# Performance work log

Measured on AMD Instinct MI355X. Metric: run time of the kernel, lower is better.

Reference implementation:

```python
import jax, jax.numpy as jnp
import numpy as np

B, N, D, H = 1, 4096, 512, 8
HD = D // H


def setup_inputs() -> dict:
    key = jax.random.key(0)
    ks = jax.random.split(key, 12)
    s = 0.02  # weight init scale for numerical stability
    query = jax.random.normal(ks[0], (B, N, D), jnp.float32)
    key_t = jax.random.normal(ks[1], (B, N, D), jnp.float32)
    value = jax.random.normal(ks[2], (B, N, D), jnp.float32)
    Wq = jax.random.normal(ks[3], (D, D), jnp.float32) * s
    bq = jax.random.normal(ks[4], (D,), jnp.float32) * s
    Wk = jax.random.normal(ks[5], (D, D), jnp.float32) * s
    bk = jax.random.normal(ks[6], (D,), jnp.float32) * s
    Wv = jax.random.normal(ks[7], (D, D), jnp.float32) * s
    bv = jax.random.normal(ks[8], (D,), jnp.float32) * s
    Wo = jax.random.normal(ks[9], (D, D), jnp.float32) * s
    bo = jax.random.normal(ks[10], (D,), jnp.float32) * s
    # build sgconv_mat exactly as __init__: shifted nonneg adjacency, max-normalized,
    # then symmetric degree normalization D^-1/2 A D^-1/2 (gwmha_layer_num=1)
    A = jax.random.uniform(ks[11], (N, N), jnp.float32)
    A = A + A.min()
    A = A / A.max()
    deg = A.sum(1)
    dinv = 1.0 / jnp.sqrt(deg)
    sgconv_mat = (dinv[:, None] * A * dinv[None, :])[None]  # [1,N,N]
    return {"query": query, "key": key_t, "value": value,
            "Wq": Wq, "bq": bq, "Wk": Wk, "bk": bk, "Wv": Wv, "bv": bv,
            "Wo": Wo, "bo": bo, "sgconv_mat": sgconv_mat}


def reference(query, key, value, Wq, bq, Wk, bk, Wv, bv, Wo, bo, sgconv_mat):
    b, n, d = query.shape
    q = (query @ Wq.T + bq).reshape(b, n, H, HD)
    k = (key @ Wk.T + bk).reshape(b, n, H, HD)
    v = (value @ Wv.T + bv).reshape(b, n, H, HD)
    energy = jnp.einsum('bqhd,bkhd->bhqk', q, k)
    attn = jax.nn.softmax(energy / jnp.sqrt(jnp.float32(d)), axis=3)
    out = jnp.einsum('bhqk,bkhd->bqhd', attn, v).reshape(b, n, d)
    out = sgconv_mat @ out          # [1,N,N] @ [B,N,D] -> [B,N,D]
    return out @ Wo.T + bo
```

## Files before the change

### kernel.cpp

```cpp
#include <hip/hip_runtime.h>
#include <hip/hip_bf16.h>
#include <math.h>

typedef __bf16 bf16_t;
typedef __bf16 bf16x8 __attribute__((ext_vector_type(8)));
typedef float floatx4 __attribute__((ext_vector_type(4)));

typedef __attribute__((address_space(1))) void gvoid_t;
typedef __attribute__((address_space(3))) void lvoid_t;

static __device__ __forceinline__ void gload_lds16(const bf16_t* g, const bf16_t* l) {
    __builtin_amdgcn_global_load_lds((gvoid_t*)(size_t)g,
                                     (lvoid_t*)(unsigned)(size_t)l,
                                     16, 0, 0);
}

static __device__ __forceinline__ unsigned pack_bf2(float lo, float hi) {
    bf16_t a = (bf16_t)lo, b = (bf16_t)hi;
    return (unsigned)__builtin_bit_cast(unsigned short, a)
         | ((unsigned)__builtin_bit_cast(unsigned short, b) << 16);
}

static __device__ inline void store_c(float* C, size_t i, float v) { C[i] = v; }
static __device__ inline void store_c(bf16_t* C, size_t i, float v) { C[i] = (bf16_t)v; }

static __device__ inline void cvt8(const float* src, bf16_t* dst, size_t idx) {
    float4 a = *(const float4*)(src + idx);
    float4 c = *(const float4*)(src + idx + 4);
    uint4 u;
    u.x = pack_bf2(a.x, a.y);
    u.y = pack_bf2(a.z, a.w);
    u.z = pack_bf2(c.x, c.y);
    u.w = pack_bf2(c.z, c.w);
    *(uint4*)(dst + idx) = u;
}

template <typename TC>
__device__ inline void gemm_body128(
    const bf16_t* __restrict__ A, int lda,
    const bf16_t* __restrict__ B, int ldb,
    const float* __restrict__ bias_col, const float* __restrict__ bias_row,
    float cscale,
    TC* __restrict__ C, int ldc, int K, int m0, int n0)
{
    __shared__ bf16_t As[128 * 32];
    __shared__ bf16_t Bs[128 * 32];

    const int tid = threadIdx.x;
    const int lane = tid & 63, wave = tid >> 6;
    const int wm = wave & 1, wn = wave >> 1;
    const int lo16 = lane & 15, quad = lane >> 4;

    const int r0 = tid >> 2;
    const int s0 = tid & 3;
    const int c0 = s0 ^ ((r0 >> 1) & 3);
    const bf16_t* ga0 = A + (size_t)(m0 + r0) * lda + c0 * 8;
    const bf16_t* ga1 = A + (size_t)(m0 + 64 + r0) * lda + c0 * 8;
    const bf16_t* gb0 = B + (size_t)(n0 + r0) * ldb + c0 * 8;
    const bf16_t* gb1 = B + (size_t)(n0 + 64 + r0) * ldb + c0 * 8;
    const bf16_t* la0 = As + wave * 512;
    const bf16_t* la1 = As + 2048 + wave * 512;
    const bf16_t* lb0 = Bs + wave * 512;
    const bf16_t* lb1 = Bs + 2048 + wave * 512;

    int aoff[4], boff[4];
#pragma unroll
    for (int t = 0; t < 4; ++t) {
        const int ra = wm * 64 + t * 16 + lo16;
        aoff[t] = ra * 32 + ((quad ^ ((ra >> 1) & 3)) << 3);
        const int rb = wn * 64 + t * 16 + lo16;
        boff[t] = rb * 32 + ((quad ^ ((rb >> 1) & 3)) << 3);
    }

    floatx4 acc[4][4] = {};

    for (int k0 = 0; k0 < K; k0 += 32) {
        __syncthreads();
        gload_lds16(ga0 + k0, la0);
        gload_lds16(ga1 + k0, la1);
        gload_lds16(gb0 + k0, lb0);
        gload_lds16(gb1 + k0, lb1);
        __syncthreads();

        bf16x8 af[4], bfv[4];
#pragma unroll
        for (int t = 0; t < 4; ++t) {
            af[t]  = *(const bf16x8*)(As + aoff[t]);
            bfv[t] = *(const bf16x8*)(Bs + boff[t]);
        }
        __builtin_amdgcn_s_setprio(1);
#pragma unroll
        for (int mt = 0; mt < 4; ++mt)
#pragma unroll
            for (int nt = 0; nt < 4; ++nt)
                acc[mt][nt] = __builtin_amdgcn_mfma_f32_16x16x32_bf16(
                    af[mt], bfv[nt], acc[mt][nt], 0, 0, 0);
        __builtin_amdgcn_s_setprio(0);
    }

#pragma unroll
    for (int nt = 0; nt < 4; ++nt) {
        const int gn = n0 + wn * 64 + nt * 16 + lo16;
        const float bc = bias_col ? bias_col[gn] : 0.f;
#pragma unroll
        for (int mt = 0; mt < 4; ++mt) {
#pragma unroll
            for (int r = 0; r < 4; ++r) {
                const int gm = m0 + wm * 64 + mt * 16 + quad * 4 + r;
                float v = acc[mt][nt][r] + bc;
                if (bias_row) v += bias_row[gm];
                store_c(C, (size_t)gm * ldc + gn, v * cscale);
            }
        }
    }
}

__global__ __launch_bounds__(256) void prep(
    const float* __restrict__ query, const float* __restrict__ key, const float* __restrict__ value,
    const float* __restrict__ Wq, const float* __restrict__ Wk,
    const float* __restrict__ Wv, const float* __restrict__ Wo,
    bf16_t* qB, bf16_t* kB, bf16_t* vB,
    bf16_t* wqB, bf16_t* wkB, bf16_t* wvB, bf16_t* woB)
{
    const int b = blockIdx.x;
    const float* src; bf16_t* dst; size_t base;
    if      (b < 256) { src = query; dst = qB;  base = (size_t)b * 8192; }
    else if (b < 512) { src = key;   dst = kB;  base = (size_t)(b - 256) * 8192; }
    else if (b < 768) { src = value; dst = vB;  base = (size_t)(b - 512) * 8192; }
    else if (b < 800) { src = Wq;    dst = wqB; base = (size_t)(b - 768) * 8192; }
    else if (b < 832) { src = Wk;    dst = wkB; base = (size_t)(b - 800) * 8192; }
    else if (b < 864) { src = Wv;    dst = wvB; base = (size_t)(b - 832) * 8192; }
    else              { src = Wo;    dst = woB; base = (size_t)(b - 864) * 8192; }
#pragma unroll
    for (int it = 0; it < 4; ++it)
        cvt8(src, dst, base + (size_t)it * 2048 + threadIdx.x * 8);
}

__global__ __launch_bounds__(256) void proj_qkv(
    const bf16_t* __restrict__ qB, const bf16_t* __restrict__ wqB, const float* __restrict__ bq,
    const bf16_t* __restrict__ kB, const bf16_t* __restrict__ wkB, const float* __restrict__ bk,
    const bf16_t* __restrict__ wvB, const bf16_t* __restrict__ vB, const float* __restrict__ bv,
    bf16_t* __restrict__ q, bf16_t* __restrict__ k, bf16_t* __restrict__ vt, float qscale,
    const float* __restrict__ sg, bf16_t* __restrict__ sgb)
{
    const int b = blockIdx.x;
    if (b >= 384) {
        const size_t base = (size_t)(b - 384) * 8192;
#pragma unroll
        for (int it = 0; it < 4; ++it)
            cvt8(sg, sgb, base + (size_t)it * 2048 + threadIdx.x * 8);
        return;
    }
    const int i = b & 127;
    if (b < 256) {
        const int m0 = (i & 31) * 128, n0 = (i >> 5) * 128;
        if (b < 128)
            gemm_body128<bf16_t>(qB, 512, wqB, 512, bq, nullptr, qscale, q, 512, 512, m0, n0);
        else
            gemm_body128<bf16_t>(kB, 512, wkB, 512, bk, nullptr, 1.f, k, 512, 512, m0, n0);
    } else {
        const int m0 = (i & 3) * 128, n0 = (i >> 2) * 128;
        gemm_body128<bf16_t>(wvB, 512, vB, 512, nullptr, bv, 1.f, vt, 4096, 512, m0, n0);
    }
}

__global__ __launch_bounds__(256) void sgconv_gemm(
    const bf16_t* __restrict__ sgb, const bf16_t* __restrict__ aot,
    float* __restrict__ part)
{
    const int i = blockIdx.x & 127;
    const int kb = blockIdx.x >> 7;
    const int m0 = (i & 31) * 128, n0 = (i >> 5) * 128;
    const int kbase = kb * 512;
    gemm_body128<float>(sgb + kbase, 4096, aot + kbase, 4096, nullptr, nullptr, 1.f,
                        part + (size_t)kb * (4096 * 512), 512, 512, m0, n0);
}

__global__ __launch_bounds__(256) void part_reduce(
    const float* __restrict__ p, bf16_t* __restrict__ o2)
{
    const size_t S = (size_t)4096 * 512;
    const size_t idx = ((size_t)blockIdx.x * 256 + threadIdx.x) * 8;
    uint4 u;
#pragma unroll
    for (int half = 0; half < 2; ++half) {
        float4 s = *(const float4*)(p + idx + half * 4);
#pragma unroll
        for (int kb = 1; kb < 8; ++kb) {
            float4 t = *(const float4*)(p + kb * S + idx + half * 4);
            s.x += t.x; s.y += t.y; s.z += t.z; s.w += t.w;
        }
        if (half == 0) { u.x = pack_bf2(s.x, s.y); u.y = pack_bf2(s.z, s.w); }
        else           { u.z = pack_bf2(s.x, s.y); u.w = pack_bf2(s.z, s.w); }
    }
    *(uint4*)(o2 + idx) = u;
}

__global__ __launch_bounds__(256) void out_proj(
    const bf16_t* __restrict__ o2, const bf16_t* __restrict__ woB,
    const float* __restrict__ bo, float* __restrict__ out)
{
    const int i = blockIdx.x, x = i & 7, t = i >> 3;
    const int n0 = (t & 7) * 64;
    const int m0 = ((t >> 3) * 8 + x) * 64;

    __shared__ bf16_t As[64 * 68];
    __shared__ bf16_t Bs[64 * 68];

    const int tid = threadIdx.x;
    const int lane = tid & 63, wave = tid >> 6;
    const int wm = wave & 1, wn = wave >> 1;
    const int lo16 = lane & 15, quad = lane >> 4;
    const int sr = tid >> 2, sc = (tid & 3) * 8;

    floatx4 acc[2][2] = {};

    for (int k0 = 0; k0 < 512; k0 += 32) {
        bf16x8 a0 = *(const bf16x8*)(o2 + (size_t)(m0 + sr) * 512 + k0 + sc);
        bf16x8 b0 = *(const bf16x8*)(woB + (size_t)(n0 + sr) * 512 + k0 + sc);
        __syncthreads();
        *(bf16x8*)(&As[sr * 68 + sc]) = a0;
        *(bf16x8*)(&Bs[sr * 68 + sc]) = b0;
        __syncthreads();

        bf16x8 af[2], bfv[2];
#pragma unroll
        for (int mt = 0; mt < 2; ++mt)
            af[mt] = *(const bf16x8*)(&As[(wm * 32 + mt * 16 + lo16) * 68 + quad * 8]);
#pragma unroll
        for (int nt = 0; nt < 2; ++nt)
            bfv[nt] = *(const bf16x8*)(&Bs[(wn * 32 + nt * 16 + lo16) * 68 + quad * 8]);
#pragma unroll
        for (int mt = 0; mt < 2; ++mt)
#pragma unroll
            for (int nt = 0; nt < 2; ++nt)
                acc[mt][nt] = __builtin_amdgcn_mfma_f32_16x16x32_bf16(
                    af[mt], bfv[nt], acc[mt][nt], 0, 0, 0);
    }

#pragma unroll
    for (int nt = 0; nt < 2; ++nt) {
        const int gn = n0 + wn * 32 + nt * 16 + lo16;
        const float bc = bo[gn];
#pragma unroll
        for (int mt = 0; mt < 2; ++mt)
#pragma unroll
            for (int r = 0; r < 4; ++r) {
                const int gm = m0 + wm * 32 + mt * 16 + quad * 4 + r;
                out[(size_t)gm * 512 + gn] = acc[mt][nt][r] + bc;
            }
    }
}

__global__ __launch_bounds__(256, 4) void flash_attn(
    const bf16_t* __restrict__ q, const bf16_t* __restrict__ kk,
    const bf16_t* __restrict__ vt, float* __restrict__ op,
    float* __restrict__ lp)
{
    const int fid = blockIdx.x;

    const int N = 4096, D = 512;
    const int h   = fid & 7;
    const int qb  = (fid >> 3) & 31;
    const int qtr = fid >> 8;
    const int t0  = qtr * 1024;

    const int tid = threadIdx.x;
    const int w = tid >> 6, lane = tid & 63;
    const int lo16 = lane & 15, quad = lane >> 4;

    __shared__ bf16_t Ks[64 * 72];
    __shared__ bf16_t Vs[64 * 72];
    __shared__ bf16_t Ps[4][32 * 72];

    const bf16_t* qp = q + (size_t)(qb * 128 + w * 32 + lo16) * D + h * 64 + quad * 8;
    bf16x8 qf[2][2];
    qf[0][0] = *(const bf16x8*)qp;
    qf[0][1] = *(const bf16x8*)(qp + 32);
    qf[1][0] = *(const bf16x8*)(qp + 16 * D);
    qf[1][1] = *(const bf16x8*)(qp + 16 * D + 32);

    const int srow = tid >> 2, sc = (tid & 3) * 16;
    const bf16_t* ksrc = kk + (size_t)(t0 + srow) * D + h * 64 + sc;
    const bf16_t* vsrc = vt + (size_t)(h * 64 + srow) * N + t0 + sc;
    bf16_t* kdst = &Ks[srow * 72 + sc];
    bf16_t* vdst = &Vs[srow * 72 + sc];

    bf16x8 ones;
#pragma unroll
    for (int i = 0; i < 8; ++i) ones[i] = (bf16_t)1.0f;

    floatx4 o[4][2] = {};
    floatx4 lacc[2] = {};

    bf16x8 kr0 = *(const bf16x8*)ksrc;
    bf16x8 kr1 = *(const bf16x8*)(ksrc + 8);
    bf16x8 vr0 = *(const bf16x8*)vsrc;
    bf16x8 vr1 = *(const bf16x8*)(vsrc + 8);

    for (int it = 0; it < 16; ++it) {
        __syncthreads();
        *(bf16x8*)kdst = kr0;  *(bf16x8*)(kdst + 8) = kr1;
        *(bf16x8*)vdst = vr0;  *(bf16x8*)(vdst + 8) = vr1;
        __syncthreads();
        if (it < 15) {
            const bf16_t* kn = ksrc + (size_t)(it + 1) * 64 * D;
            const bf16_t* vn = vsrc + (it + 1) * 64;
            kr0 = *(const bf16x8*)kn;  kr1 = *(const bf16x8*)(kn + 8);
            vr0 = *(const bf16x8*)vn;  vr1 = *(const bf16x8*)(vn + 8);
        }

        floatx4 s[4][2];
        __builtin_amdgcn_s_setprio(1);
#pragma unroll
        for (int tt = 0; tt < 4; ++tt) {
            bf16x8 kf0 = *(const bf16x8*)(&Ks[(tt * 16 + lo16) * 72 + quad * 8]);
            bf16x8 kf1 = *(const bf16x8*)(&Ks[(tt * 16 + lo16) * 72 + 32 + quad * 8]);
#pragma unroll
            for (int qt = 0; qt < 2; ++qt) {
                floatx4 a = {};
                a = __builtin_amdgcn_mfma_f32_16x16x32_bf16(kf0, qf[qt][0], a, 0, 0, 0);
                a = __builtin_amdgcn_mfma_f32_16x16x32_bf16(kf1, qf[qt][1], a, 0, 0, 0);
                s[tt][qt] = a;
            }
        }
        __builtin_amdgcn_s_setprio(0);
#pragma unroll
        for (int tt = 0; tt < 4; ++tt)
#pragma unroll
            for (int qt = 0; qt < 2; ++qt) {
                float e0 = __builtin_amdgcn_exp2f(s[tt][qt][0]);
                float e1 = __builtin_amdgcn_exp2f(s[tt][qt][1]);
                float e2 = __builtin_amdgcn_exp2f(s[tt][qt][2]);
                float e3 = __builtin_amdgcn_exp2f(s[tt][qt][3]);
                uint2 pk;
                pk.x = pack_bf2(e0, e1);
                pk.y = pack_bf2(e2, e3);
                *(uint2*)(&Ps[w][(qt * 16 + lo16) * 72 + tt * 16 + quad * 4]) = pk;
            }
        __builtin_amdgcn_s_setprio(1);
#pragma unroll
        for (int ks = 0; ks < 2; ++ks) {
            bf16x8 pf0 = *(const bf16x8*)(&Ps[w][lo16 * 72 + ks * 32 + quad * 8]);
            bf16x8 pf1 = *(const bf16x8*)(&Ps[w][(16 + lo16) * 72 + ks * 32 + quad * 8]);
            lacc[0] = __builtin_amdgcn_mfma_f32_16x16x32_bf16(ones, pf0, lacc[0], 0, 0, 0);
            lacc[1] = __builtin_amdgcn_mfma_f32_16x16x32_bf16(ones, pf1, lacc[1], 0, 0, 0);
#pragma unroll
            for (int t = 0; t < 4; ++t) {
                bf16x8 vf = *(const bf16x8*)(&Vs[(t * 16 + lo16) * 72 + ks * 32 + quad * 8]);
                o[t][0] = __builtin_amdgcn_mfma_f32_16x16x32_bf16(vf, pf0, o[t][0], 0, 0, 0);
                o[t][1] = __builtin_amdgcn_mfma_f32_16x16x32_bf16(vf, pf1, o[t][1], 0, 0, 0);
            }
        }
        __builtin_amdgcn_s_setprio(0);
    }

    const int g = fid & 255;
    float* opw = op + ((size_t)qtr * 256 + g) * 8192;
#pragma unroll
    for (int t = 0; t < 4; ++t)
#pragma unroll
        for (int pt = 0; pt < 2; ++pt)
#pragma unroll
            for (int r = 0; r < 4; ++r)
                opw[(t * 16 + quad * 4 + r) * 128 + w * 32 + pt * 16 + lo16] = o[t][pt][r];

    if (quad == 0) {
        float* lpw = lp + ((size_t)qtr * 256 + g) * 128;
        lpw[w * 32 + lo16] = lacc[0][0];
        lpw[w * 32 + 16 + lo16] = lacc[1][0];
    }
}

__global__ __launch_bounds__(256) void attn_combine(
    const float* __restrict__ op, const float* __restrict__ lp, bf16_t* __restrict__ aot)
{
    const int bid = blockIdx.x;
    const int g = bid >> 2, qu = bid & 3;
    const int h = g & 7, qb = g >> 3;
    const int tid = threadIdx.x;
    __shared__ float ls[128];
    if (tid < 128) {
        float s = 0.f;
#pragma unroll
        for (int qtr = 0; qtr < 4; ++qtr)
            s += lp[((size_t)qtr * 256 + g) * 128 + tid];
        ls[tid] = 1.0f / s;
    }
    __syncthreads();
    const float* b0 = op + (size_t)g * 8192;
    const size_t QS = (size_t)256 * 8192;
#pragma unroll
    for (int i = 0; i < 8; ++i) {
        int idx = qu * 2048 + i * 256 + tid;
        float v = b0[idx] + b0[QS + idx] + b0[2 * QS + idx] + b0[3 * QS + idx];
        int dim = idx >> 7, qc = idx & 127;
        aot[(size_t)(h * 64 + dim) * 4096 + qb * 128 + qc] = (bf16_t)(v * ls[qc]);
    }
}

extern "C" void kernel_launch(void* const* d_in, const int* in_sizes, int n_in,
                              void* d_out, int out_size, void* d_ws, size_t ws_size,
                              hipStream_t stream)
{
    const int N = 4096, D = 512;
    const float* query = (const float*)d_in[0];
    const float* key_t = (const float*)d_in[1];
    const float* value = (const float*)d_in[2];
    const float* Wq = (const float*)d_in[3];
    const float* bq = (const float*)d_in[4];
    const float* Wk = (const float*)d_in[5];
    const float* bk = (const float*)d_in[6];
    const float* Wv = (const float*)d_in[7];
    const float* bv = (const float*)d_in[8];
    const float* Wo = (const float*)d_in[9];
    const float* bo = (const float*)d_in[10];
    const float* sg = (const float*)d_in[11];
    float* out = (float*)d_out;

    const size_t ND = (size_t)N * D;
    const size_t DD = (size_t)D * D;

    char* base = (char*)d_ws;
    bf16_t* q    = (bf16_t*)base;
    bf16_t* kk   = q   + ND;
    bf16_t* vt   = kk  + ND;
    bf16_t* aot  = vt  + ND;
    bf16_t* sgb  = aot + ND;
    char* regA   = (char*)(sgb + (size_t)N * N);
    bf16_t* qB   = (bf16_t*)regA;
    bf16_t* kB   = qB + ND;
    bf16_t* vB   = kB + ND;
    bf16_t* wqB  = vB + ND;
    bf16_t* wkB  = wqB + DD;
    bf16_t* wvB  = wkB + DD;
    float* op    = (float*)regA;
    float* p     = (float*)regA;
    char* tail   = regA + (size_t)8 * (4096 * 512) * 4;
    float*  lp   = (float*)tail;
    bf16_t* woB  = (bf16_t*)(lp + (size_t)4 * 256 * 128);
    bf16_t* o2   = woB + DD;

    const dim3 blk(256);

    prep<<<896, blk, 0, stream>>>(query, key_t, value, Wq, Wk, Wv, Wo,
                                  qB, kB, vB, wqB, wkB, wvB, woB);

    const float qscale = 1.44269504088896f / sqrtf((float)D);
    proj_qkv<<<2432, blk, 0, stream>>>(qB, wqB, bq, kB, wkB, bk,
                                       wvB, vB, bv, q, kk, vt, qscale, sg, sgb);

    flash_attn<<<1024, blk, 0, stream>>>(q, kk, vt, op, lp);
    attn_combine<<<1024, blk, 0, stream>>>(op, lp, aot);

    sgconv_gemm<<<1024, blk, 0, stream>>>(sgb, aot, p);
    part_reduce<<<1024, blk, 0, stream>>>(p, o2);
    out_proj<<<512, blk, 0, stream>>>(o2, woB, bo, out);

    (void)in_sizes; (void)n_in; (void)out_size; (void)ws_size;
}
```

Before: 261.3 us.

## Replace split-K sgconv GEMM and reduction with single full-K 64x64 kernel

The sgconv matmul used to be split-K over 8 slices. Each slice wrote fp32 partials and a separate reduce kernel summed them. It is now one kernel per 64x64 output tile that loops over the full K=4096 with XOR-swizzled LDS tiles and writes bf16 directly. This removes the 8x fp32 partial write and readback and one launch, at the cost of 512 longer-running blocks with less parallelism per tile. The setprio hints around the MFMA sections in the GEMM body and flash attention are also removed.

```diff
diff --git a/kernel.cpp b/kernel.cpp
--- a/kernel.cpp
+++ b/kernel.cpp
@@ -88,14 +88,12 @@
             af[t]  = *(const bf16x8*)(As + aoff[t]);
             bfv[t] = *(const bf16x8*)(Bs + boff[t]);
         }
-        __builtin_amdgcn_s_setprio(1);
 #pragma unroll
         for (int mt = 0; mt < 4; ++mt)
 #pragma unroll
             for (int nt = 0; nt < 4; ++nt)
                 acc[mt][nt] = __builtin_amdgcn_mfma_f32_16x16x32_bf16(
                     af[mt], bfv[nt], acc[mt][nt], 0, 0, 0);
-        __builtin_amdgcn_s_setprio(0);
     }
 
 #pragma unroll
@@ -164,36 +162,81 @@
     }
 }
 
-__global__ __launch_bounds__(256) void sgconv_gemm(
+__global__ __launch_bounds__(256) void sgconv_full(
     const bf16_t* __restrict__ sgb, const bf16_t* __restrict__ aot,
-    float* __restrict__ part)
-{
-    const int i = blockIdx.x & 127;
-    const int kb = blockIdx.x >> 7;
-    const int m0 = (i & 31) * 128, n0 = (i >> 5) * 128;
-    const int kbase = kb * 512;
-    gemm_body128<float>(sgb + kbase, 4096, aot + kbase, 4096, nullptr, nullptr, 1.f,
-                        part + (size_t)kb * (4096 * 512), 512, 512, m0, n0);
-}
-
-__global__ __launch_bounds__(256) void part_reduce(
-    const float* __restrict__ p, bf16_t* __restrict__ o2)
-{
-    const size_t S = (size_t)4096 * 512;
-    const size_t idx = ((size_t)blockIdx.x * 256 + threadIdx.x) * 8;
-    uint4 u;
-#pragma unroll
-    for (int half = 0; half < 2; ++half) {
-        float4 s = *(const float4*)(p + idx + half * 4);
-#pragma unroll
-        for (int kb = 1; kb < 8; ++kb) {
-            float4 t = *(const float4*)(p + kb * S + idx + half * 4);
-            s.x += t.x; s.y += t.y; s.z += t.z; s.w += t.w;
-        }
-        if (half == 0) { u.x = pack_bf2(s.x, s.y); u.y = pack_bf2(s.z, s.w); }
-        else           { u.z = pack_bf2(s.x, s.y); u.w = pack_bf2(s.z, s.w); }
-    }
-    *(uint4*)(o2 + idx) = u;
+    bf16_t* __restrict__ o2)
+{
+    const int i = blockIdx.x;
+    const int m0 = (i & 63) * 64;
+    const int n0 = (i >> 6) * 64;
+
+    __shared__ bf16_t As[64 * 64];
+    __shared__ bf16_t Bs[64 * 64];
+
+    const int tid = threadIdx.x;
+    const int lane = tid & 63, wave = tid >> 6;
+    const int wm = wave & 1, wn = wave >> 1;
+    const int lo16 = lane & 15, quad = lane >> 4;
+
+    const int r0 = tid >> 3, s0 = tid & 7;
+    const int c0 = s0 ^ (r0 & 7);
+    const bf16_t* gaA = sgb + (size_t)(m0 + r0) * 4096 + c0 * 8;
+    const bf16_t* gaB = aot + (size_t)(n0 + r0) * 4096 + c0 * 8;
+    const bf16_t* laA0 = As + wave * 512;
+    const bf16_t* laA1 = As + 2048 + wave * 512;
+    const bf16_t* laB0 = Bs + wave * 512;
+    const bf16_t* laB1 = Bs + 2048 + wave * 512;
+
+    int aoff[2][2], boff[2][2];
+#pragma unroll
+    for (int t = 0; t < 2; ++t)
+#pragma unroll
+        for (int kk = 0; kk < 2; ++kk) {
+            const int ra = wm * 32 + t * 16 + lo16;
+            aoff[t][kk] = ra * 64 + (((kk * 4 + quad) ^ (ra & 7)) << 3);
+            const int rb = wn * 32 + t * 16 + lo16;
+            boff[t][kk] = rb * 64 + (((kk * 4 + quad) ^ (rb & 7)) << 3);
+        }
+
+    floatx4 acc[2][2] = {};
+
+    for (int k0 = 0; k0 < 4096; k0 += 64) {
+        __syncthreads();
+        gload_lds16(gaA + k0, laA0);
+        gload_lds16(gaA + (size_t)32 * 4096 + k0, laA1);
+        gload_lds16(gaB + k0, laB0);
+        gload_lds16(gaB + (size_t)32 * 4096 + k0, laB1);
+        __syncthreads();
+
+        bf16x8 af[2][2], bfv[2][2];
+#pragma unroll
+        for (int t = 0; t < 2; ++t)
+#pragma unroll
+            for (int kk = 0; kk < 2; ++kk) {
+                af[t][kk]  = *(const bf16x8*)(As + aoff[t][kk]);
+                bfv[t][kk] = *(const bf16x8*)(Bs + boff[t][kk]);
+            }
+#pragma unroll
+        for (int mt = 0; mt < 2; ++mt)
+#pragma unroll
+            for (int nt = 0; nt < 2; ++nt)
+#pragma unroll
+                for (int kk = 0; kk < 2; ++kk)
+                    acc[mt][nt] = __builtin_amdgcn_mfma_f32_16x16x32_bf16(
+                        af[mt][kk], bfv[nt][kk], acc[mt][nt], 0, 0, 0);
+    }
+
+#pragma unroll
+    for (int nt = 0; nt < 2; ++nt) {
+        const int gn = n0 + wn * 32 + nt * 16 + lo16;
+#pragma unroll
+        for (int mt = 0; mt < 2; ++mt)
+#pragma unroll
+            for (int r = 0; r < 4; ++r) {
+                const int gm = m0 + wm * 32 + mt * 16 + quad * 4 + r;
+                o2[(size_t)gm * 512 + gn] = (bf16_t)acc[mt][nt][r];
+            }
+    }
 }
 
 __global__ __launch_bounds__(256) void out_proj(
@@ -311,7 +354,6 @@
         }
 
         floatx4 s[4][2];
-        __builtin_amdgcn_s_setprio(1);
 #pragma unroll
         for (int tt = 0; tt < 4; ++tt) {
             bf16x8 kf0 = *(const bf16x8*)(&Ks[(tt * 16 + lo16) * 72 + quad * 8]);
@@ -324,7 +366,6 @@
                 s[tt][qt] = a;
             }
         }
-        __builtin_amdgcn_s_setprio(0);
 #pragma unroll
         for (int tt = 0; tt < 4; ++tt)
 #pragma unroll
@@ -338,7 +379,6 @@
                 pk.y = pack_bf2(e2, e3);
                 *(uint2*)(&Ps[w][(qt * 16 + lo16) * 72 + tt * 16 + quad * 4]) = pk;
             }
-        __builtin_amdgcn_s_setprio(1);
 #pragma unroll
         for (int ks = 0; ks < 2; ++ks) {
             bf16x8 pf0 = *(const bf16x8*)(&Ps[w][lo16 * 72 + ks * 32 + quad * 8]);
@@ -352,7 +392,6 @@
                 o[t][1] = __builtin_amdgcn_mfma_f32_16x16x32_bf16(vf, pf1, o[t][1], 0, 0, 0);
             }
         }
-        __builtin_amdgcn_s_setprio(0);
     }
 
     const int g = fid & 255;
@@ -435,8 +474,7 @@
     bf16_t* wkB  = wqB + DD;
     bf16_t* wvB  = wkB + DD;
     float* op    = (float*)regA;
-    float* p     = (float*)regA;
-    char* tail   = regA + (size_t)8 * (4096 * 512) * 4;
+    char* tail   = regA + (size_t)4 * 256 * 8192 * 4;
     float*  lp   = (float*)tail;
     bf16_t* woB  = (bf16_t*)(lp + (size_t)4 * 256 * 128);
     bf16_t* o2   = woB + DD;
@@ -453,8 +491,7 @@
     flash_attn<<<1024, blk, 0, stream>>>(q, kk, vt, op, lp);
     attn_combine<<<1024, blk, 0, stream>>>(op, lp, aot);
 
-    sgconv_gemm<<<1024, blk, 0, stream>>>(sgb, aot, p);
-    part_reduce<<<1024, blk, 0, stream>>>(p, o2);
+    sgconv_full<<<512, blk, 0, stream>>>(sgb, aot, o2);
     out_proj<<<512, blk, 0, stream>>>(o2, woB, bo, out);
 
     (void)in_sizes; (void)n_in; (void)out_size; (void)ws_size;
```

After: 256.7 us. No clear change (-1.8%).
